# Optimization experiments

Hardware: AMD Instinct MI355X
Metric: run time of the kernel (lower is better)

The kernel has to match this reference:

```python
import jax, jax.numpy as jnp
import numpy as np

B, T, C, H = 2, 2048, 1024, 16
HD = C // H
EPS = 1e-5


def setup_inputs() -> dict:
    key = jax.random.key(0)
    ks = jax.random.split(key, 16)
    s = 0.02
    return {
        "x": jax.random.normal(ks[0], (B, T, C), jnp.float32),
        "ln1_w": jnp.ones((C,), jnp.float32),
        "ln1_b": jnp.zeros((C,), jnp.float32),
        "ln2_w": jnp.ones((C,), jnp.float32),
        "ln2_b": jnp.zeros((C,), jnp.float32),
        "Wq": jax.random.normal(ks[1], (C, C), jnp.float32) * s,
        "bq": jnp.zeros((C,), jnp.float32),
        "Wk": jax.random.normal(ks[2], (C, C), jnp.float32) * s,
        "bk": jnp.zeros((C,), jnp.float32),
        "Wv": jax.random.normal(ks[3], (C, C), jnp.float32) * s,
        "bv": jnp.zeros((C,), jnp.float32),
        "Wp": jax.random.normal(ks[4], (C, C), jnp.float32) * s,
        "bp": jnp.zeros((C,), jnp.float32),
        "W1": jax.random.normal(ks[5], (4 * C, C), jnp.float32) * s,
        "b1": jnp.zeros((4 * C,), jnp.float32),
        "W2": jax.random.normal(ks[6], (C, 4 * C), jnp.float32) * s,
        "b2": jnp.zeros((C,), jnp.float32),
    }


def _ln(x, w, b):
    mu = jnp.mean(x, axis=-1, keepdims=True)
    var = jnp.mean((x - mu) ** 2, axis=-1, keepdims=True)
    return (x - mu) * jax.lax.rsqrt(var + EPS) * w + b


def _heads(t):  # (B,T,C) -> (B,H,T,HD)
    return t.reshape(B, T, H, HD).transpose(0, 2, 1, 3)


def reference(x, ln1_w, ln1_b, ln2_w, ln2_b, Wq, bq, Wk, bk, Wv, bv, Wp, bp, W1, b1, W2, b2):
    h = _ln(x, ln1_w, ln1_b)
    q = _heads(h @ Wq.T + bq)
    k = _heads(h @ Wk.T + bk)
    v = _heads(h @ Wv.T + bv)
    att = jnp.einsum("bhqd,bhkd->bhqk", q, k) * (1.0 / np.sqrt(HD))
    causal = jnp.tril(jnp.ones((T, T), bool))
    att = jnp.where(causal, att, -jnp.inf)
    att = jax.nn.softmax(att, axis=-1)
    y = jnp.einsum("bhqk,bhkd->bhqd", att, v)
    y = y.transpose(0, 2, 1, 3).reshape(B, T, C)
    x = x + (y @ Wp.T + bp)
    h2 = _ln(x, ln2_w, ln2_b)
    m = jax.nn.gelu(h2 @ W1.T + b1, approximate=False)
    x = x + (m @ W2.T + b2)
    return x
```

## Files before the change

kernel.cpp:

```cpp
#include <hip/hip_runtime.h>

#define TB 2
#define TT 2048
#define TC 1024
#define TH 16
#define THD 64
#define LNEPS 1e-5f

typedef _Float16 f16;
typedef __attribute__((ext_vector_type(8))) _Float16 f16x8;
typedef __attribute__((ext_vector_type(4))) _Float16 f16x4;
typedef __attribute__((ext_vector_type(4))) float f32x4;

__device__ __forceinline__ f32x4 mfma_16x16x32(f16x8 a, f16x8 b, f32x4 c) {
    return __builtin_amdgcn_mfma_f32_16x16x32_f16(a, b, c, 0, 0, 0);
}

__device__ __forceinline__ void load_lds16(const f16* g, f16* l) {
    __builtin_amdgcn_global_load_lds(
        (const __attribute__((address_space(1))) unsigned int*)g,
        (__attribute__((address_space(3))) unsigned int*)l, 16, 0, 0);
}

__device__ __forceinline__ float gelu_fast(float v) {
    float u = 0.7978845608f * v * (1.f + 0.044715f * v * v);
    float e = __expf(2.f * u);
    return v - v / (e + 1.f);
}

__global__ __launch_bounds__(256) void ln_kernel(const float* __restrict__ x,
                                                 const float* __restrict__ w,
                                                 const float* __restrict__ bsrc,
                                                 f16* __restrict__ out) {
    int row  = blockIdx.x * 4 + (threadIdx.x >> 6);
    int lane = threadIdx.x & 63;
    const float4* xr = (const float4*)(x + (size_t)row * TC);
    float4 v[4];
    float s = 0.f, ss = 0.f;
#pragma unroll
    for (int i = 0; i < 4; i++) {
        v[i] = xr[i * 64 + lane];
        s  += v[i].x + v[i].y + v[i].z + v[i].w;
        ss += v[i].x * v[i].x + v[i].y * v[i].y + v[i].z * v[i].z + v[i].w * v[i].w;
    }
#pragma unroll
    for (int off = 32; off > 0; off >>= 1) {
        s  += __shfl_xor(s, off);
        ss += __shfl_xor(ss, off);
    }
    float mean = s * (1.f / TC);
    float var  = ss * (1.f / TC) - mean * mean;
    float rstd = rsqrtf(var + LNEPS);
    const float4* wv = (const float4*)w;
    const float4* bv = (const float4*)bsrc;
    f16x4* ov = (f16x4*)(out + (size_t)row * TC);
#pragma unroll
    for (int i = 0; i < 4; i++) {
        int idx = i * 64 + lane;
        float4 wc = wv[idx], bc = bv[idx];
        f16x4 o;
        o[0] = (f16)((v[i].x - mean) * rstd * wc.x + bc.x);
        o[1] = (f16)((v[i].y - mean) * rstd * wc.y + bc.y);
        o[2] = (f16)((v[i].z - mean) * rstd * wc.z + bc.z);
        o[3] = (f16)((v[i].w - mean) * rstd * wc.w + bc.w);
        ov[idx] = o;
    }
}

__global__ __launch_bounds__(256) void prep_kernel(
    const float* __restrict__ Wq, const float* __restrict__ Wk,
    const float* __restrict__ Wv, const float* __restrict__ Wp,
    const float* __restrict__ W1, const float* __restrict__ W2,
    f16* __restrict__ dst,
    const float* __restrict__ x, const float* __restrict__ lnw,
    const float* __restrict__ lnb, f16* __restrict__ out) {
    int bid = blockIdx.x;
    if (bid < 12288) {
        int i = bid * 256 + threadIdx.x;
        const int Q = 262144;
        const float* src;
        int j;
        int s = i >> 18;
        if (s < 4) {
            src = (s == 0) ? Wq : (s == 1) ? Wk : (s == 2) ? Wv : Wp;
            j = i & (Q - 1);
        } else if (s < 8) {
            src = W1; j = i - 4 * Q;
        } else {
            src = W2; j = i - 8 * Q;
        }
        float4 v = ((const float4*)src)[j];
        f16x4 o;
        o[0] = (f16)v.x; o[1] = (f16)v.y; o[2] = (f16)v.z; o[3] = (f16)v.w;
        ((f16x4*)dst)[i] = o;
    } else {
        int row  = (bid - 12288) * 4 + (threadIdx.x >> 6);
        int lane = threadIdx.x & 63;
        const float4* xr = (const float4*)(x + (size_t)row * TC);
        float4 v[4];
        float s = 0.f, ss = 0.f;
#pragma unroll
        for (int i = 0; i < 4; i++) {
            v[i] = xr[i * 64 + lane];
            s  += v[i].x + v[i].y + v[i].z + v[i].w;
            ss += v[i].x * v[i].x + v[i].y * v[i].y + v[i].z * v[i].z + v[i].w * v[i].w;
        }
#pragma unroll
        for (int off = 32; off > 0; off >>= 1) {
            s  += __shfl_xor(s, off);
            ss += __shfl_xor(ss, off);
        }
        float mean = s * (1.f / TC);
        float var  = ss * (1.f / TC) - mean * mean;
        float rstd = rsqrtf(var + LNEPS);
        const float4* wv = (const float4*)lnw;
        const float4* bv = (const float4*)lnb;
        f16x4* ov = (f16x4*)(out + (size_t)row * TC);
#pragma unroll
        for (int i = 0; i < 4; i++) {
            int idx = i * 64 + lane;
            float4 wc = wv[idx], bc = bv[idx];
            f16x4 o;
            o[0] = (f16)((v[i].x - mean) * rstd * wc.x + bc.x);
            o[1] = (f16)((v[i].y - mean) * rstd * wc.y + bc.y);
            o[2] = (f16)((v[i].z - mean) * rstd * wc.z + bc.z);
            o[3] = (f16)((v[i].w - mean) * rstd * wc.w + bc.w);
            ov[idx] = o;
        }
    }
}

template <int BM, int BN, int BK, int EPI>
__global__ __launch_bounds__(256) void gemm_kernel(const f16* __restrict__ A,
                                                   const f16* __restrict__ W,
                                                   const float* __restrict__ bias,
                                                   const float* __restrict__ bias2,
                                                   const float* __restrict__ bias3,
                                                   const float* __restrict__ res,
                                                   void* __restrict__ outp,
                                                   int M, int N, int K) {
    constexpr int CPR = BK / 8;
    __shared__ __align__(16) f16 sA[BM * BK];
    __shared__ __align__(16) f16 sB[BN * BK];
    const int t  = threadIdx.x;
    const int m0 = blockIdx.y * BM;
    const int n0 = blockIdx.x * BN;
    const int wid = t >> 6, lane = t & 63;
    const int wr = wid >> 1, wc = wid & 1;
    constexpr int WM = BM / 2, WN = BN / 2;
    constexpr int MI = WM / 16, NI = WN / 16;
    f32x4 acc[MI][NI];
#pragma unroll
    for (int i = 0; i < MI; i++)
#pragma unroll
        for (int j = 0; j < NI; j++) acc[i][j] = (f32x4){0.f, 0.f, 0.f, 0.f};
    const int quad = lane >> 4, l15 = lane & 15;

    for (int k0 = 0; k0 < K; k0 += BK) {
#pragma unroll
        for (int i = 0; i < BM * CPR / 256; i++) {
            int p = t + i * 256;
            int row = p / CPR, pc = p % CPR;
            int c = (pc - (row >> 1)) & (CPR - 1);
            load_lds16(&A[(size_t)(m0 + row) * K + k0 + c * 8], &sA[p * 8]);
        }
#pragma unroll
        for (int i = 0; i < BN * CPR / 256; i++) {
            int p = t + i * 256;
            int row = p / CPR, pc = p % CPR;
            int c = (pc - (row >> 1)) & (CPR - 1);
            load_lds16(&W[(size_t)(n0 + row) * K + k0 + c * 8], &sB[p * 8]);
        }
        __syncthreads();
#pragma unroll
        for (int ks = 0; ks < BK / 32; ks++) {
            f16x8 af[MI], bf[NI];
#pragma unroll
            for (int i = 0; i < MI; i++) {
                int r = wr * WM + i * 16 + l15;
                af[i] = *(const f16x8*)&sA[(r * CPR + ((ks * 4 + quad + (r >> 1)) & (CPR - 1))) * 8];
            }
#pragma unroll
            for (int j = 0; j < NI; j++) {
                int r = wc * WN + j * 16 + l15;
                bf[j] = *(const f16x8*)&sB[(r * CPR + ((ks * 4 + quad + (r >> 1)) & (CPR - 1))) * 8];
            }
#pragma unroll
            for (int i = 0; i < MI; i++)
#pragma unroll
                for (int j = 0; j < NI; j++)
                    acc[i][j] = mfma_16x16x32(af[i], bf[j], acc[i][j]);
        }
        __syncthreads();
    }

#pragma unroll
    for (int i = 0; i < MI; i++) {
#pragma unroll
        for (int j = 0; j < NI; j++) {
            int col   = n0 + wc * WN + j * 16 + l15;
            int rbase = m0 + wr * WM + i * 16 + quad * 4;
            float bvv = bias ? bias[col] : 0.f;
#pragma unroll
            for (int r = 0; r < 4; r++) {
                size_t idx = (size_t)(rbase + r) * N + col;
                float v = acc[i][j][r] + bvv;
                if constexpr (EPI == 1) {
                    ((float*)outp)[idx] = v + res[idx];
                } else {
                    ((f16*)outp)[idx] = (f16)v;
                }
            }
        }
    }
}

#define BARF() do { __builtin_amdgcn_s_barrier(); asm volatile("" ::: "memory"); } while (0)

template <int EPI>
__global__ __launch_bounds__(512, 2) void gemm256_kernel(
    const f16* __restrict__ A, const f16* __restrict__ W,
    const float* __restrict__ bias, const float* __restrict__ bias2,
    const float* __restrict__ bias3,
    f16* __restrict__ out0, f16* __restrict__ out1,
    f16* __restrict__ out2, f16* __restrict__ out3,
    int M, int N, int K) {
    __shared__ __align__(16) f16 lds[8 * 8192];
    f16* sA = lds;
    f16* sB = lds + 4 * 8192;
    const int t    = threadIdx.x;
    const int lane = t & 63, wid = t >> 6;
    const int quad = lane >> 4, l15 = lane & 15;
    const int wr = wid >> 2, wc = wid & 3;
    const int m0 = blockIdx.y * 256, n0 = blockIdx.x * 256;
    int kbeg = 0, nsub = K >> 5;
    f16* outp = out0;
    if constexpr (EPI == 4) {
        int Kc = K >> 2;
        kbeg = blockIdx.z * Kc;
        nsub = Kc >> 5;
        outp = (blockIdx.z == 0) ? out0 : (blockIdx.z == 1) ? out1
             : (blockIdx.z == 2) ? out2 : out3;
    }
    const f16* Abase = A + (size_t)m0 * K + kbeg;
    const f16* Wbase = W + (size_t)n0 * K + kbeg;

    int srow[2], sgo[2], sld[2];
#pragma unroll
    for (int i = 0; i < 2; i++) {
        int p = t + i * 512;
        int r = p >> 2;
        srow[i] = r;
        sgo[i]  = (((p & 3) - (r >> 1)) & 3) * 8;
        sld[i]  = p * 8;
    }
    auto stageA = [&](int s) {
        if (s >= nsub) return;
        f16* dst = sA + (s & 3) * 8192;
        const f16* src = Abase + s * 32;
#pragma unroll
        for (int i = 0; i < 2; i++)
            load_lds16(src + (size_t)srow[i] * K + sgo[i], dst + sld[i]);
    };
    auto stageB = [&](int s) {
        if (s >= nsub) return;
        f16* dst = sB + (s & 3) * 8192;
        const f16* src = Wbase + s * 32;
#pragma unroll
        for (int i = 0; i < 2; i++)
            load_lds16(src + (size_t)srow[i] * K + sgo[i], dst + sld[i]);
    };

    int offA[8], offB[4];
#pragma unroll
    for (int q = 0; q < 8; q++) {
        int row = wr * 128 + q * 16 + l15;
        offA[q] = row * 32 + (((quad + (row >> 1)) & 3) * 8);
    }
#pragma unroll
    for (int q = 0; q < 4; q++) {
        int row = wc * 64 + q * 16 + l15;
        offB[q] = row * 32 + (((quad + (row >> 1)) & 3) * 8);
    }

    f32x4 acc[8][4];
#pragma unroll
    for (int i = 0; i < 8; i++)
#pragma unroll
        for (int j = 0; j < 4; j++) acc[i][j] = (f32x4){0.f, 0.f, 0.f, 0.f};

    stageA(0); stageB(0); stageA(1); stageB(1); stageA(2); stageB(2);
    asm volatile("s_waitcnt vmcnt(8)" ::: "memory");
    BARF();

    for (int s = 0; s < nsub; s += 2) {
#pragma unroll
        for (int h = 0; h < 2; h++) {
            const int su = s + h;
            const f16* slA = sA + (su & 3) * 8192;
            const f16* slB = sB + (su & 3) * 8192;
            f16x8 af[4], bf[4];
#pragma unroll
            for (int q = 0; q < 4; q++) af[q] = *(const f16x8*)&slA[offA[q]];
#pragma unroll
            for (int q = 0; q < 4; q++) bf[q] = *(const f16x8*)&slB[offB[q]];
            stageA(su + 3);
            __builtin_amdgcn_s_barrier();
            asm volatile("s_waitcnt lgkmcnt(0)" ::: "memory");
            __builtin_amdgcn_s_setprio(1);
#pragma unroll
            for (int i = 0; i < 4; i++)
#pragma unroll
                for (int j = 0; j < 4; j++)
                    acc[i][j] = mfma_16x16x32(af[i], bf[j], acc[i][j]);
            __builtin_amdgcn_s_setprio(0);
            asm volatile("" ::: "memory");
            BARF();
#pragma unroll
            for (int q = 0; q < 4; q++) af[q] = *(const f16x8*)&slA[offA[4 + q]];
            stageB(su + 3);
            __builtin_amdgcn_s_barrier();
            asm volatile("s_waitcnt lgkmcnt(0)" ::: "memory");
            __builtin_amdgcn_s_setprio(1);
#pragma unroll
            for (int i = 0; i < 4; i++)
#pragma unroll
                for (int j = 0; j < 4; j++)
                    acc[4 + i][j] = mfma_16x16x32(af[i], bf[j], acc[4 + i][j]);
            __builtin_amdgcn_s_setprio(0);
            if (su + 3 < nsub)      asm volatile("s_waitcnt vmcnt(8)" ::: "memory");
            else if (su + 2 < nsub) asm volatile("s_waitcnt vmcnt(4)" ::: "memory");
            else                    asm volatile("s_waitcnt vmcnt(0)" ::: "memory");
            BARF();
        }
    }

#pragma unroll
    for (int fr = 0; fr < 8; fr++) {
#pragma unroll
        for (int fc = 0; fc < 4; fc++) {
            int col   = n0 + wc * 64 + fc * 16 + l15;
            int rbase = m0 + wr * 128 + fr * 16 + quad * 4;
            float bvv = 0.f;
            if constexpr (EPI == 3)
                bvv = (col < 1024) ? bias[col]
                    : (col < 2048) ? bias2[col - 1024] : bias3[col - 2048];
            else if constexpr (EPI == 2)
                bvv = bias[col];
#pragma unroll
            for (int r = 0; r < 4; r++) {
                size_t idx = (size_t)(rbase + r) * N + col;
                float v = acc[fr][fc][r] + bvv;
                if constexpr (EPI == 2) outp[idx] = (f16)gelu_fast(v);
                else                    outp[idx] = (f16)v;
            }
        }
    }
}

__global__ __launch_bounds__(256) void reduce4_kernel(const f16* __restrict__ p0,
                                                      const f16* __restrict__ p1,
                                                      const f16* __restrict__ p2,
                                                      const f16* __restrict__ p3,
                                                      const float* __restrict__ b2,
                                                      float* __restrict__ x1) {
    int i = blockIdx.x * 256 + threadIdx.x;
    f16x4 a = ((const f16x4*)p0)[i], b = ((const f16x4*)p1)[i];
    f16x4 c = ((const f16x4*)p2)[i], d = ((const f16x4*)p3)[i];
    float4 r = ((float4*)x1)[i];
    float4 bb = ((const float4*)b2)[i & 255];
    r.x += (float)a[0] + (float)b[0] + (float)c[0] + (float)d[0] + bb.x;
    r.y += (float)a[1] + (float)b[1] + (float)c[1] + (float)d[1] + bb.y;
    r.z += (float)a[2] + (float)b[2] + (float)c[2] + (float)d[2] + bb.z;
    r.w += (float)a[3] + (float)b[3] + (float)c[3] + (float)d[3] + bb.w;
    ((float4*)x1)[i] = r;
}

__global__ __launch_bounds__(256) void transpose_kernel(const f16* __restrict__ in,
                                                        f16* __restrict__ out) {
    __shared__ f16 tile[32][33];
    int bt = blockIdx.x;
    int b  = bt / (TT / 32);
    int t0 = (bt % (TT / 32)) * 32;
    int c0 = blockIdx.y * 32;
    int tx = threadIdx.x & 31;
    int ty = threadIdx.x >> 5;
    for (int r = ty; r < 32; r += 8)
        tile[r][tx] = in[(size_t)(b * TT + t0 + r) * 3072 + 2048 + c0 + tx];
    __syncthreads();
    for (int r = ty; r < 32; r += 8)
        out[(size_t)(b * TC + c0 + r) * TT + t0 + tx] = tile[tx][r];
}

__global__ __launch_bounds__(256, 4) void attn_kernel(const f16* __restrict__ qkv,
                                                      const f16* __restrict__ vtg,
                                                      f16* __restrict__ yg,
                                                      int qbase) {
    __shared__ __align__(16) f16 sK[2][64 * 64];
    __shared__ __align__(16) f16 sV[2][64 * 64];
    __shared__ __align__(16) f16 pl[4][16 * 64];
    const int t    = threadIdx.x;
    const int wid  = t >> 6, lane = t & 63;
    const int quad = lane >> 4, l15 = lane & 15;
    const int idx = blockIdx.x;
    const int bh = idx & 31;
    const int qi = idx >> 5;
    const int qblk = qbase + ((qi < 8) ? qi : 23 - qi);
    const int b = bh >> 4, h = bh & 15;
    const int q0 = qblk * 64;
    const int q0w = q0 + wid * 16;

    const f16* qptr = qkv + (size_t)(b * TT) * 3072 + h * THD;
    const f16* kptr = qptr + 1024;

    f16x8 qa0, qa1;
    {
        const f16* qb_ = qptr + (size_t)(q0w + l15) * 3072 + quad * 8;
        qa0 = *(const f16x8*)qb_;
        qa1 = *(const f16x8*)(qb_ + 32);
#pragma unroll
        for (int j = 0; j < 8; j++) { qa0[j] *= (f16)0.125f; qa1[j] *= (f16)0.125f; }
    }

    auto stage = [&](int buf, int k0) {
#pragma unroll
        for (int i = 0; i < 2; i++) {
            int p = t + i * 256;
            int row = p >> 3, c0 = p & 7;
            int cc = c0 ^ (row & 7);
            load_lds16(kptr + (size_t)(k0 + row) * 3072 + cc * 8, &sK[buf][p * 8]);
            load_lds16(vtg + (size_t)(bh * THD + row) * TT + k0 + cc * 8, &sV[buf][p * 8]);
        }
    };

    f32x4 o[4];
#pragma unroll
    for (int j = 0; j < 4; j++) o[j] = (f32x4){0.f, 0.f, 0.f, 0.f};
    float mcol = -__builtin_inff(), lsum = 0.f;
    f16* plw = pl[wid];
    const int sw = (l15 & 7) << 1;
    const int nt = qblk + 1;

    stage(0, 0);
    for (int it = 0; it < nt; it++) {
        const int cur = it & 1;
        __syncthreads();
        if (it + 1 < nt) stage(cur ^ 1, (it + 1) * 64);
        const int k0 = it * 64;
        if (k0 <= q0w + 15) {
            const f16* sk = sK[cur];
            f32x4 s[4];
#pragma unroll
            for (int g = 0; g < 4; g++) {
                int key = g * 16 + l15;
                f16x8 klo = *(const f16x8*)&sk[(key * 8 + (quad ^ (l15 & 7))) * 8];
                f16x8 khi = *(const f16x8*)&sk[(key * 8 + ((quad + 4) ^ (l15 & 7))) * 8];
                f32x4 a = (f32x4){0.f, 0.f, 0.f, 0.f};
                a = mfma_16x16x32(klo, qa0, a);
                a = mfma_16x16x32(khi, qa1, a);
                s[g] = a;
            }
            const bool full = (k0 + 63 <= q0w);
            float lm = -__builtin_inff();
#pragma unroll
            for (int g = 0; g < 4; g++) {
#pragma unroll
                for (int rr = 0; rr < 4; rr++) {
                    if (!full) {
                        int key = k0 + g * 16 + quad * 4 + rr;
                        if (key > q0w + l15) s[g][rr] = -__builtin_inff();
                    }
                    lm = fmaxf(lm, s[g][rr]);
                }
            }
            lm = fmaxf(lm, __shfl_xor(lm, 16));
            lm = fmaxf(lm, __shfl_xor(lm, 32));
            float mnew  = fmaxf(mcol, lm);
            float alpha = __expf(mcol - mnew);
            mcol = mnew;
            float sum = 0.f;
#pragma unroll
            for (int g = 0; g < 4; g++) {
                f16x4 pw;
#pragma unroll
                for (int rr = 0; rr < 4; rr++) {
                    float p = __expf(s[g][rr] - mnew);
                    sum += p;
                    pw[rr] = (f16)p;
                }
                *(f16x4*)&plw[(l15 * 16 + ((g * 4 + quad) ^ sw)) * 4] = pw;
            }
            sum += __shfl_xor(sum, 16);
            sum += __shfl_xor(sum, 32);
            lsum = lsum * alpha + sum;
#pragma unroll
            for (int j = 0; j < 4; j++) {
                o[j][0] *= alpha; o[j][1] *= alpha; o[j][2] *= alpha; o[j][3] *= alpha;
            }
            __asm__ volatile("s_waitcnt lgkmcnt(0)" ::: "memory");
            const f16* sv = sV[cur];
#pragma unroll
            for (int hh = 0; hh < 2; hh++) {
                f16x8 pb = *(const f16x8*)&plw[(l15 * 16 + ((hh * 8 + quad * 2) ^ sw)) * 4];
#pragma unroll
                for (int j = 0; j < 4; j++) {
                    int d = j * 16 + l15;
                    f16x8 vf = *(const f16x8*)&sv[(d * 8 + ((4 * hh + quad) ^ (l15 & 7))) * 8];
                    o[j] = mfma_16x16x32(vf, pb, o[j]);
                }
            }
        }
    }
    float inv = 1.f / lsum;
    size_t rowbase = (size_t)(b * TT + q0w + l15) * TC + h * THD;
#pragma unroll
    for (int j = 0; j < 4; j++) {
        f16x4 ov;
#pragma unroll
        for (int rr = 0; rr < 4; rr++) ov[rr] = (f16)(o[j][rr] * inv);
        *(f16x4*)&yg[rowbase + j * 16 + quad * 4] = ov;
    }
}

extern "C" void kernel_launch(void* const* d_in, const int* in_sizes, int n_in,
                              void* d_out, int out_size, void* d_ws, size_t ws_size,
                              hipStream_t stream) {
    const float* x    = (const float*)d_in[0];
    const float* ln1w = (const float*)d_in[1];
    const float* ln1b = (const float*)d_in[2];
    const float* ln2w = (const float*)d_in[3];
    const float* ln2b = (const float*)d_in[4];
    const float* Wq   = (const float*)d_in[5];
    const float* bq   = (const float*)d_in[6];
    const float* Wk   = (const float*)d_in[7];
    const float* bk   = (const float*)d_in[8];
    const float* Wv   = (const float*)d_in[9];
    const float* bv   = (const float*)d_in[10];
    const float* Wp   = (const float*)d_in[11];
    const float* bp   = (const float*)d_in[12];
    const float* W1   = (const float*)d_in[13];
    const float* b1   = (const float*)d_in[14];
    const float* W2   = (const float*)d_in[15];
    const float* b2   = (const float*)d_in[16];

    char* ws = (char*)d_ws;
    const size_t MB = 1024 * 1024;
    f16* hb   = (f16*)(ws + 0);
    f16* qkv  = (f16*)(ws + 8 * MB);
    f16* vT   = (f16*)(ws + 32 * MB);
    f16* mb   = (f16*)(ws + 16 * MB);
    f16* Wb   = (f16*)(ws + 48 * MB);
    f16* Wqb  = Wb;
    f16* Wpb  = Wb + (size_t)3 * 1024 * 1024;
    f16* W1b  = Wb + (size_t)4 * 1024 * 1024;
    f16* W2b  = Wb + (size_t)8 * 1024 * 1024;
    f16* yb   = hb;
    f16* h2b  = qkv;
    f16* part0 = (f16*)(ws + 0);
    f16* part1 = (f16*)(ws + 8 * MB);
    f16* part2 = (f16*)(ws + 48 * MB);
    f16* part3 = (f16*)(ws + 56 * MB);
    float* x1 = (float*)d_out;

    prep_kernel<<<13312, 256, 0, stream>>>(Wq, Wk, Wv, Wp, W1, W2, Wb,
                                           x, ln1w, ln1b, hb);

    gemm256_kernel<3><<<dim3(3072 / 256, (TB * TT) / 256), 512, 0, stream>>>(
        hb, Wqb, bq, bk, bv, qkv, nullptr, nullptr, nullptr, TB * TT, 3072, TC);
    transpose_kernel<<<dim3(TB * TT / 32, TC / 32), 256, 0, stream>>>(qkv, vT);
    attn_kernel<<<512, 256, 0, stream>>>(qkv, vT, yb, 0);
    attn_kernel<<<512, 256, 0, stream>>>(qkv, vT, yb, 16);
    gemm_kernel<128, 64, 64, 1><<<dim3(TC / 64, (TB * TT) / 128), 256, 0, stream>>>(
        yb, Wpb, bp, nullptr, nullptr, x, x1, TB * TT, TC, TC);
    ln_kernel<<<1024, 256, 0, stream>>>(x1, ln2w, ln2b, h2b);
    gemm256_kernel<2><<<dim3(4 * TC / 256, (TB * TT) / 256), 512, 0, stream>>>(
        h2b, W1b, b1, nullptr, nullptr, mb, nullptr, nullptr, nullptr, TB * TT, 4 * TC, TC);
    gemm256_kernel<4><<<dim3(TC / 256, (TB * TT) / 256, 4), 512, 0, stream>>>(
        mb, W2b, nullptr, nullptr, nullptr, part0, part1, part2, part3, TB * TT, TC, 4 * TC);
    reduce4_kernel<<<4096, 256, 0, stream>>>(part0, part1, part2, part3, b2, x1);
}
```

Baseline: 366.3 us.

## Shrink GEMM tile to 256x128 with 3-stage pipeline and merge attention launches

The large GEMM kernel moves from a 256x256 tile with a 4-deep LDS ring to a 256x128 tile with a 3-deep ring. Each warp now holds a 64x64 accumulator, which allows up to 4 blocks per CU and gives a simpler single-phase K loop with one barrier pair per step. The grids double along N. Separately, the two attention launches are merged into one 1024-block launch that pairs heavy and light causal query blocks for load balance. The smaller tile lowers operand reuse per LDS byte and issues more global loads in exchange for higher occupancy and more blocks to spread across CUs.

```diff
diff --git a/kernel.cpp b/kernel.cpp
--- a/kernel.cpp
+++ b/kernel.cpp
@@ -218,21 +218,21 @@
 #define BARF() do { __builtin_amdgcn_s_barrier(); asm volatile("" ::: "memory"); } while (0)
 
 template <int EPI>
-__global__ __launch_bounds__(512, 2) void gemm256_kernel(
+__global__ __launch_bounds__(512, 4) void gemm256_kernel(
     const f16* __restrict__ A, const f16* __restrict__ W,
     const float* __restrict__ bias, const float* __restrict__ bias2,
     const float* __restrict__ bias3,
     f16* __restrict__ out0, f16* __restrict__ out1,
     f16* __restrict__ out2, f16* __restrict__ out3,
     int M, int N, int K) {
-    __shared__ __align__(16) f16 lds[8 * 8192];
+    __shared__ __align__(16) f16 lds[3 * 8192 + 3 * 4096];
     f16* sA = lds;
-    f16* sB = lds + 4 * 8192;
+    f16* sB = lds + 3 * 8192;
     const int t    = threadIdx.x;
     const int lane = t & 63, wid = t >> 6;
     const int quad = lane >> 4, l15 = lane & 15;
-    const int wr = wid >> 2, wc = wid & 3;
-    const int m0 = blockIdx.y * 256, n0 = blockIdx.x * 256;
+    const int wr = wid >> 1, wc = wid & 1;
+    const int m0 = blockIdx.y * 256, n0 = blockIdx.x * 128;
     int kbeg = 0, nsub = K >> 5;
     f16* outp = out0;
     if constexpr (EPI == 4) {
@@ -245,36 +245,38 @@
     const f16* Abase = A + (size_t)m0 * K + kbeg;
     const f16* Wbase = W + (size_t)n0 * K + kbeg;
 
-    int srow[2], sgo[2], sld[2];
+    int arow[2], ago[2], ald[2], brow, bgo, bld;
 #pragma unroll
     for (int i = 0; i < 2; i++) {
         int p = t + i * 512;
         int r = p >> 2;
-        srow[i] = r;
-        sgo[i]  = (((p & 3) - (r >> 1)) & 3) * 8;
-        sld[i]  = p * 8;
-    }
-    auto stageA = [&](int s) {
+        arow[i] = r;
+        ago[i]  = (((p & 3) - (r >> 1)) & 3) * 8;
+        ald[i]  = p * 8;
+    }
+    {
+        int r = t >> 2;
+        brow = r;
+        bgo  = (((t & 3) - (r >> 1)) & 3) * 8;
+        bld  = t * 8;
+    }
+    auto stage = [&](int s) {
         if (s >= nsub) return;
-        f16* dst = sA + (s & 3) * 8192;
-        const f16* src = Abase + s * 32;
+        int sl = s % 3;
+        f16* dA = sA + sl * 8192;
+        f16* dB = sB + sl * 4096;
+        const f16* srcA = Abase + s * 32;
+        const f16* srcB = Wbase + s * 32;
 #pragma unroll
         for (int i = 0; i < 2; i++)
-            load_lds16(src + (size_t)srow[i] * K + sgo[i], dst + sld[i]);
+            load_lds16(srcA + (size_t)arow[i] * K + ago[i], dA + ald[i]);
+        load_lds16(srcB + (size_t)brow * K + bgo, dB + bld);
     };
-    auto stageB = [&](int s) {
-        if (s >= nsub) return;
-        f16* dst = sB + (s & 3) * 8192;
-        const f16* src = Wbase + s * 32;
-#pragma unroll
-        for (int i = 0; i < 2; i++)
-            load_lds16(src + (size_t)srow[i] * K + sgo[i], dst + sld[i]);
-    };
-
-    int offA[8], offB[4];
-#pragma unroll
-    for (int q = 0; q < 8; q++) {
-        int row = wr * 128 + q * 16 + l15;
+
+    int offA[4], offB[4];
+#pragma unroll
+    for (int q = 0; q < 4; q++) {
+        int row = wr * 64 + q * 16 + l15;
         offA[q] = row * 32 + (((quad + (row >> 1)) & 3) * 8);
     }
 #pragma unroll
@@ -283,64 +285,45 @@
         offB[q] = row * 32 + (((quad + (row >> 1)) & 3) * 8);
     }
 
-    f32x4 acc[8][4];
-#pragma unroll
-    for (int i = 0; i < 8; i++)
+    f32x4 acc[4][4];
+#pragma unroll
+    for (int i = 0; i < 4; i++)
 #pragma unroll
         for (int j = 0; j < 4; j++) acc[i][j] = (f32x4){0.f, 0.f, 0.f, 0.f};
 
-    stageA(0); stageB(0); stageA(1); stageB(1); stageA(2); stageB(2);
-    asm volatile("s_waitcnt vmcnt(8)" ::: "memory");
+    stage(0); stage(1);
+    asm volatile("s_waitcnt vmcnt(3)" ::: "memory");
     BARF();
 
-    for (int s = 0; s < nsub; s += 2) {
-#pragma unroll
-        for (int h = 0; h < 2; h++) {
-            const int su = s + h;
-            const f16* slA = sA + (su & 3) * 8192;
-            const f16* slB = sB + (su & 3) * 8192;
-            f16x8 af[4], bf[4];
-#pragma unroll
-            for (int q = 0; q < 4; q++) af[q] = *(const f16x8*)&slA[offA[q]];
-#pragma unroll
-            for (int q = 0; q < 4; q++) bf[q] = *(const f16x8*)&slB[offB[q]];
-            stageA(su + 3);
-            __builtin_amdgcn_s_barrier();
-            asm volatile("s_waitcnt lgkmcnt(0)" ::: "memory");
-            __builtin_amdgcn_s_setprio(1);
-#pragma unroll
-            for (int i = 0; i < 4; i++)
-#pragma unroll
-                for (int j = 0; j < 4; j++)
-                    acc[i][j] = mfma_16x16x32(af[i], bf[j], acc[i][j]);
-            __builtin_amdgcn_s_setprio(0);
-            asm volatile("" ::: "memory");
-            BARF();
-#pragma unroll
-            for (int q = 0; q < 4; q++) af[q] = *(const f16x8*)&slA[offA[4 + q]];
-            stageB(su + 3);
-            __builtin_amdgcn_s_barrier();
-            asm volatile("s_waitcnt lgkmcnt(0)" ::: "memory");
-            __builtin_amdgcn_s_setprio(1);
-#pragma unroll
-            for (int i = 0; i < 4; i++)
-#pragma unroll
-                for (int j = 0; j < 4; j++)
-                    acc[4 + i][j] = mfma_16x16x32(af[i], bf[j], acc[4 + i][j]);
-            __builtin_amdgcn_s_setprio(0);
-            if (su + 3 < nsub)      asm volatile("s_waitcnt vmcnt(8)" ::: "memory");
-            else if (su + 2 < nsub) asm volatile("s_waitcnt vmcnt(4)" ::: "memory");
-            else                    asm volatile("s_waitcnt vmcnt(0)" ::: "memory");
-            BARF();
-        }
-    }
-
-#pragma unroll
-    for (int fr = 0; fr < 8; fr++) {
+    for (int su = 0; su < nsub; ++su) {
+        const f16* slA = sA + (su % 3) * 8192;
+        const f16* slB = sB + (su % 3) * 4096;
+        f16x8 af[4], bf[4];
+#pragma unroll
+        for (int q = 0; q < 4; q++) bf[q] = *(const f16x8*)&slB[offB[q]];
+#pragma unroll
+        for (int q = 0; q < 4; q++) af[q] = *(const f16x8*)&slA[offA[q]];
+        stage(su + 2);
+        __builtin_amdgcn_s_barrier();
+        __builtin_amdgcn_s_setprio(1);
+#pragma unroll
+        for (int i = 0; i < 4; i++)
+#pragma unroll
+            for (int j = 0; j < 4; j++)
+                acc[i][j] = mfma_16x16x32(af[i], bf[j], acc[i][j]);
+        __builtin_amdgcn_s_setprio(0);
+        __builtin_amdgcn_sched_barrier(0);
+        if (su + 2 < nsub) asm volatile("s_waitcnt vmcnt(3)" ::: "memory");
+        else               asm volatile("s_waitcnt vmcnt(0)" ::: "memory");
+        BARF();
+    }
+
+#pragma unroll
+    for (int fr = 0; fr < 4; fr++) {
 #pragma unroll
         for (int fc = 0; fc < 4; fc++) {
             int col   = n0 + wc * 64 + fc * 16 + l15;
-            int rbase = m0 + wr * 128 + fr * 16 + quad * 4;
+            int rbase = m0 + wr * 64 + fr * 16 + quad * 4;
             float bvv = 0.f;
             if constexpr (EPI == 3)
                 bvv = (col < 1024) ? bias[col]
@@ -394,8 +377,7 @@
 
 __global__ __launch_bounds__(256, 4) void attn_kernel(const f16* __restrict__ qkv,
                                                       const f16* __restrict__ vtg,
-                                                      f16* __restrict__ yg,
-                                                      int qbase) {
+                                                      f16* __restrict__ yg) {
     __shared__ __align__(16) f16 sK[2][64 * 64];
     __shared__ __align__(16) f16 sV[2][64 * 64];
     __shared__ __align__(16) f16 pl[4][16 * 64];
@@ -403,9 +385,9 @@
     const int wid  = t >> 6, lane = t & 63;
     const int quad = lane >> 4, l15 = lane & 15;
     const int idx = blockIdx.x;
-    const int bh = idx & 31;
-    const int qi = idx >> 5;
-    const int qblk = qbase + ((qi < 8) ? qi : 23 - qi);
+    const int u = idx & 255, r = idx >> 8;
+    const int bh = u & 31, rc = u >> 5;
+    const int qblk = (r == 0) ? rc : (r == 1) ? 31 - rc : (r == 2) ? 8 + rc : 23 - rc;
     const int b = bh >> 4, h = bh & 15;
     const int q0 = qblk * 64;
     const int q0w = q0 + wid * 16;
@@ -565,17 +547,16 @@
     prep_kernel<<<13312, 256, 0, stream>>>(Wq, Wk, Wv, Wp, W1, W2, Wb,
                                            x, ln1w, ln1b, hb);
 
-    gemm256_kernel<3><<<dim3(3072 / 256, (TB * TT) / 256), 512, 0, stream>>>(
+    gemm256_kernel<3><<<dim3(3072 / 128, (TB * TT) / 256), 512, 0, stream>>>(
         hb, Wqb, bq, bk, bv, qkv, nullptr, nullptr, nullptr, TB * TT, 3072, TC);
     transpose_kernel<<<dim3(TB * TT / 32, TC / 32), 256, 0, stream>>>(qkv, vT);
-    attn_kernel<<<512, 256, 0, stream>>>(qkv, vT, yb, 0);
-    attn_kernel<<<512, 256, 0, stream>>>(qkv, vT, yb, 16);
+    attn_kernel<<<1024, 256, 0, stream>>>(qkv, vT, yb);
     gemm_kernel<128, 64, 64, 1><<<dim3(TC / 64, (TB * TT) / 128), 256, 0, stream>>>(
         yb, Wpb, bp, nullptr, nullptr, x, x1, TB * TT, TC, TC);
     ln_kernel<<<1024, 256, 0, stream>>>(x1, ln2w, ln2b, h2b);
-    gemm256_kernel<2><<<dim3(4 * TC / 256, (TB * TT) / 256), 512, 0, stream>>>(
+    gemm256_kernel<2><<<dim3(4 * TC / 128, (TB * TT) / 256), 512, 0, stream>>>(
         h2b, W1b, b1, nullptr, nullptr, mb, nullptr, nullptr, nullptr, TB * TT, 4 * TC, TC);
-    gemm256_kernel<4><<<dim3(TC / 256, (TB * TT) / 256, 4), 512, 0, stream>>>(
+    gemm256_kernel<4><<<dim3(TC / 128, (TB * TT) / 256, 4), 512, 0, stream>>>(
         mb, W2b, nullptr, nullptr, nullptr, part0, part1, part2, part3, TB * TT, TC, 4 * TC);
     reduce4_kernel<<<4096, 256, 0, stream>>>(part0, part1, part2, part3, b2, x1);
 }
```

Measured after the change: 370.9 us. About the same (+1.3%).
